# Optimization experiments

Hardware: AMD Instinct MI355X
Metric: run time of the kernel (lower is better)

The kernel has to match this reference:

```python
import jax, jax.numpy as jnp
import numpy as np
import math

B, H, S, D = 8, 16, 1024, 64


def setup_inputs() -> dict:
    key = jax.random.key(0)
    kq, kk, kv, kl = jax.random.split(key, 4)
    queries = jax.random.normal(kq, (B * H, S, D), dtype=jnp.float32)
    keys = jax.random.normal(kk, (B * H, S, D), dtype=jnp.float32)
    values = jax.random.normal(kv, (B * H, S, D), dtype=jnp.float32)
    valid_lens = jax.random.randint(kl, (B,), 0, 1024, dtype=jnp.int64)
    return {"queries": queries, "keys": keys, "values": values, "valid_lens": valid_lens}


def reference(queries, keys, values, valid_lens):
    d = queries.shape[-1]
    seq_len = queries.shape[1]
    b = valid_lens.shape[0]
    h = queries.shape[0] // b
    scale = 1.0 / math.sqrt(d)
    # [BH, S, S] scores, faithful to bmm(q, k^T)/sqrt(d)
    scores = jnp.einsum("bqd,bkd->bqk", queries, keys) * scale
    # encode_mask: mask[b, q, k] = (k >= valid_lens[b]) for 1-D valid_lens
    key_mask = jnp.arange(seq_len) >= valid_lens[:, None]  # [B, S]
    scores = scores.reshape(b, h, seq_len, seq_len)
    # masked_fill with 1e-6 (NOT -inf), faithful to the original
    scores = jnp.where(key_mask[:, None, None, :], jnp.float32(1e-6), scores)
    attn = jax.nn.softmax(scores, axis=-1)
    out = jnp.einsum("bhqk,bhkd->bhqd", attn, values.reshape(b, h, seq_len, d))
    return out.reshape(b * h, seq_len, d)
```

## Files before the change

kernel.cpp:

```cpp
#include <hip/hip_runtime.h>
#include <hip/hip_bf16.h>

typedef short short4v __attribute__((ext_vector_type(4)));
typedef short short8v __attribute__((ext_vector_type(8)));
typedef float floatx4 __attribute__((ext_vector_type(4)));

#define SLEN 1024
#define DDIM 64
#define NBH  128
#define PSTR 72

__device__ __forceinline__ unsigned short f2bf(float f) {
  union { float f; unsigned int u; } v; v.f = f;
  unsigned int u = v.u;
  u += 0x7fffu + ((u >> 16) & 1u);
  return (unsigned short)(u >> 16);
}

__device__ __forceinline__ unsigned int pkbf(float a, float b) {
  __hip_bfloat162 h = __float22bfloat162_rn(float2{a, b});
  union { __hip_bfloat162 h; unsigned int u; } c; c.h = h;
  return c.u;
}

__device__ __forceinline__ int decode_vl(const int* __restrict__ vraw, int bh) {
  const bool is64 = (vraw[1] == 0) && (vraw[3] == 0) && (vraw[5] == 0) && (vraw[7] == 0);
  const int b = bh >> 4;
  return is64 ? vraw[2 * b] : vraw[b];
}

__global__ __launch_bounds__(64)
void prep_cs(const float* __restrict__ Vg, float* __restrict__ CS,
             const int* __restrict__ vraw) {
  const int tile = blockIdx.x;
  const int bh = tile >> 4, ch = tile & 15;
  const int d = threadIdx.x;
  const int vl = decode_vl(vraw, bh);
  const int ts = (vl >> 6) + ((vl & 63) ? 1 : 0);
  float sum = 0.f;
  if (ch >= ts) {
    const float* src = Vg + (size_t)(bh * SLEN + ch * 64) * DDIM + d;
    float s0 = 0.f, s1 = 0.f, s2 = 0.f, s3 = 0.f;
    #pragma unroll
    for (int k = 0; k < 64; k += 4) {
      s0 += src[(size_t)(k + 0) * DDIM];
      s1 += src[(size_t)(k + 1) * DDIM];
      s2 += src[(size_t)(k + 2) * DDIM];
      s3 += src[(size_t)(k + 3) * DDIM];
    }
    sum = (s0 + s1) + (s2 + s3);
  }
  CS[(size_t)tile * 64 + d] = sum;
}

__global__ __launch_bounds__(64)
void prep_sv(float* __restrict__ CS, const int* __restrict__ vraw, int* __restrict__ SRT) {
  const int blk = blockIdx.x;
  if (blk < NBH) {
    const int d = threadIdx.x;
    float acc = 0.f;
    for (int ch = 15; ch >= 0; --ch) {
      const size_t idx = ((size_t)blk * 16 + ch) * 64 + d;
      acc += CS[idx];
      CS[idx] = acc;
    }
  } else {
    const int x = threadIdx.x;
    if (x < 8) {
      int key[16];
      #pragma unroll
      for (int k = 0; k < 16; ++k) {
        const int vv = decode_vl(vraw, x + 8 * k);
        key[k] = (vv >> 6) + ((vv & 63) ? 1 : 0);
      }
      #pragma unroll
      for (int i = 0; i < 16; ++i) {
        int rank = 0;
        #pragma unroll
        for (int k2 = 0; k2 < 16; ++k2)
          rank += (int)((key[k2] > key[i]) || (key[k2] == key[i] && k2 < i));
        SRT[x * 16 + rank] = x + 8 * i;
      }
    }
  }
}

__global__ __launch_bounds__(256)
void attn_main(const float* __restrict__ Qg, const float* __restrict__ Kg,
               const float* __restrict__ Vg, const float* __restrict__ SV,
               const int* __restrict__ SRT, const int* __restrict__ vraw,
               float* __restrict__ Og)
{
  __shared__ unsigned short K_lds[2][4096];
  __shared__ unsigned short VT_lds[2][4096];
  __shared__ unsigned short P_lds[4][32 * PSTR];

  const int t  = threadIdx.x;
  const int w  = t >> 6;
  const int ln = t & 15;
  const int g  = (t >> 4) & 3;

  int bh, q0;
  if (SRT) {
    const int xcd  = blockIdx.x & 7;
    const int lidx = blockIdx.x >> 3;
    const int cu   = lidx & 31;
    const int j    = lidx >> 5;
    const int r    = j * 32 + ((j & 1) ? (31 - cu) : cu);
    bh = SRT[xcd * 16 + (r >> 3)];
    q0 = (r & 7) * 128;
  } else {
    bh = blockIdx.x & 127;
    q0 = (blockIdx.x >> 7) * 128;
  }

  const int vl          = decode_vl(vraw, bh);
  const int full_ch     = vl >> 6;
  const int has_partial = (vl & 63) ? 1 : 0;
  const int nch         = SV ? (full_ch + has_partial) : 16;
  const int tail_start  = full_ch + has_partial;

  const float qs = 0.125f * 1.44269504f;
  short8v bq[2][2];
  #pragma unroll
  for (int nt = 0; nt < 2; ++nt) {
    const float* qp = Qg + ((size_t)bh * SLEN + q0 + w * 32 + nt * 16 + ln) * DDIM;
    #pragma unroll
    for (int st = 0; st < 2; ++st) {
      const float4 f0 = *(const float4*)(qp + st * 32 + g * 8);
      const float4 f1 = *(const float4*)(qp + st * 32 + g * 8 + 4);
      short8v a;
      a[0]=(short)f2bf(f0.x*qs); a[1]=(short)f2bf(f0.y*qs);
      a[2]=(short)f2bf(f0.z*qs); a[3]=(short)f2bf(f0.w*qs);
      a[4]=(short)f2bf(f1.x*qs); a[5]=(short)f2bf(f1.y*qs);
      a[6]=(short)f2bf(f1.z*qs); a[7]=(short)f2bf(f1.w*qs);
      bq[nt][st] = a;
    }
  }

  const int l7  = ln & 7;
  const int sw0 = ((g) ^ l7) * 8;
  const int sw1 = ((4 + g) ^ l7) * 8;

  short8v ones;
  #pragma unroll
  for (int j = 0; j < 8; ++j) ones[j] = (short)0x3F80;

  floatx4 o[2][4], lacc[2];
  #pragma unroll
  for (int m = 0; m < 2; ++m) {
    lacc[m] = (floatx4){0.f, 0.f, 0.f, 0.f};
    #pragma unroll
    for (int f = 0; f < 4; ++f) o[m][f] = (floatx4){0.f, 0.f, 0.f, 0.f};
  }

  float kr[2][8];
  float vlo[8], vhi[8];
  const int dv = t & 31;
  const int gv = t >> 5;

  const float* kbB = Kg + (size_t)bh * SLEN * DDIM;
  const float* vbB = Vg + (size_t)bh * SLEN * DDIM;

  auto stage_load = [&](int ch) {
    const float* kb_ = kbB + (size_t)ch * 64 * DDIM;
    const float* vb_ = vbB + (size_t)ch * 64 * DDIM;
    #pragma unroll
    for (int h = 0; h < 2; ++h) {
      const int q = t + h * 256;
      const int r = q >> 3, gr = q & 7;
      const float4 f0 = *(const float4*)(kb_ + r * DDIM + gr * 8);
      const float4 f1 = *(const float4*)(kb_ + r * DDIM + gr * 8 + 4);
      kr[h][0]=f0.x; kr[h][1]=f0.y; kr[h][2]=f0.z; kr[h][3]=f0.w;
      kr[h][4]=f1.x; kr[h][5]=f1.y; kr[h][6]=f1.z; kr[h][7]=f1.w;
    }
    #pragma unroll
    for (int j = 0; j < 8; ++j) {
      vlo[j] = vb_[(gv * 8 + j) * DDIM + dv];
      vhi[j] = vb_[(gv * 8 + j) * DDIM + dv + 32];
    }
  };
  auto stage_write = [&](int b) {
    #pragma unroll
    for (int h = 0; h < 2; ++h) {
      const int q = t + h * 256;
      const int r = q >> 3, gr = q & 7;
      union { short8v s; unsigned int u[4]; } ks;
      ks.u[0] = pkbf(kr[h][0], kr[h][1]);
      ks.u[1] = pkbf(kr[h][2], kr[h][3]);
      ks.u[2] = pkbf(kr[h][4], kr[h][5]);
      ks.u[3] = pkbf(kr[h][6], kr[h][7]);
      *(short8v*)&K_lds[b][r * 64 + ((gr ^ (r & 7)) * 8)] = ks.s;
    }
    union { short8v s; unsigned int u[4]; } va, vb2;
    va.u[0]  = pkbf(vlo[0], vlo[1]); va.u[1]  = pkbf(vlo[2], vlo[3]);
    va.u[2]  = pkbf(vlo[4], vlo[5]); va.u[3]  = pkbf(vlo[6], vlo[7]);
    vb2.u[0] = pkbf(vhi[0], vhi[1]); vb2.u[1] = pkbf(vhi[2], vhi[3]);
    vb2.u[2] = pkbf(vhi[4], vhi[5]); vb2.u[3] = pkbf(vhi[6], vhi[7]);
    const int swv = (gv ^ (dv & 7)) * 8;
    *(short8v*)&VT_lds[b][dv * 64 + swv] = va.s;
    *(short8v*)&VT_lds[b][(dv + 32) * 64 + swv] = vb2.s;
  };

  if (nch > 0) {
    stage_load(0);
    stage_write(0);
    if (nch > 1) stage_load(1);
    asm volatile("s_waitcnt lgkmcnt(0)" ::: "memory");
    __builtin_amdgcn_s_barrier();
    asm volatile("" ::: "memory");
  }

  for (int ch = 0; ch < nch; ++ch) {
    const int b = ch & 1;
    if (ch + 1 < nch) stage_write(b ^ 1);
    if (ch + 2 < nch) stage_load(ch + 2);

    floatx4 c[4][2];
    __builtin_amdgcn_s_setprio(1);
    #pragma unroll
    for (int mt = 0; mt < 4; ++mt) {
      const short8v a0 = *(const short8v*)&K_lds[b][(mt * 16 + ln) * 64 + sw0];
      const short8v a1 = *(const short8v*)&K_lds[b][(mt * 16 + ln) * 64 + sw1];
      #pragma unroll
      for (int nt = 0; nt < 2; ++nt) {
        floatx4 acc = (floatx4){0.f, 0.f, 0.f, 0.f};
        acc = __builtin_amdgcn_mfma_f32_16x16x32_bf16(a0, bq[nt][0], acc, 0, 0, 0);
        acc = __builtin_amdgcn_mfma_f32_16x16x32_bf16(a1, bq[nt][1], acc, 0, 0, 0);
        c[mt][nt] = acc;
      }
    }
    __builtin_amdgcn_s_setprio(0);

    const bool fullv = (ch < full_ch);
    #pragma unroll
    for (int mt = 0; mt < 4; ++mt) {
      const int kg = ch * 64 + mt * 16 + g * 4;
      #pragma unroll
      for (int nt = 0; nt < 2; ++nt) {
        float p[4];
        if (fullv) {
          #pragma unroll
          for (int i = 0; i < 4; ++i) p[i] = __builtin_amdgcn_exp2f(c[mt][nt][i]);
        } else {
          #pragma unroll
          for (int i = 0; i < 4; ++i) {
            const float x = (kg + i < vl) ? c[mt][nt][i] : 0.0f;
            p[i] = __builtin_amdgcn_exp2f(x);
          }
        }
        union { short4v v; unsigned int u[2]; } pk;
        pk.u[0] = pkbf(p[0], p[1]);
        pk.u[1] = pkbf(p[2], p[3]);
        *(short4v*)&P_lds[w][(nt * 16 + ln) * PSTR + mt * 16 + g * 4] = pk.v;
      }
    }

    #pragma unroll
    for (int st = 0; st < 2; ++st) {
      const short8v ap0 = *(const short8v*)&P_lds[w][(ln)      * PSTR + st * 32 + g * 8];
      const short8v ap1 = *(const short8v*)&P_lds[w][(16 + ln) * PSTR + st * 32 + g * 8];
      __builtin_amdgcn_s_setprio(1);
      lacc[0] = __builtin_amdgcn_mfma_f32_16x16x32_bf16(ap0, ones, lacc[0], 0, 0, 0);
      lacc[1] = __builtin_amdgcn_mfma_f32_16x16x32_bf16(ap1, ones, lacc[1], 0, 0, 0);
      const int sw = (st == 0) ? sw0 : sw1;
      #pragma unroll
      for (int f = 0; f < 4; ++f) {
        const short8v bv = *(const short8v*)&VT_lds[b][(f * 16 + ln) * 64 + sw];
        o[0][f] = __builtin_amdgcn_mfma_f32_16x16x32_bf16(ap0, bv, o[0][f], 0, 0, 0);
        o[1][f] = __builtin_amdgcn_mfma_f32_16x16x32_bf16(ap1, bv, o[1][f], 0, 0, 0);
      }
      __builtin_amdgcn_s_setprio(0);
    }

    if (ch + 1 < nch) {
      asm volatile("s_waitcnt lgkmcnt(0)" ::: "memory");
      __builtin_amdgcn_s_barrier();
      asm volatile("" ::: "memory");
    }
  }

  if (SV != nullptr && tail_start < 16) {
    const float* sv = SV + ((size_t)bh * 16 + tail_start) * 64;
    float svf[4];
    #pragma unroll
    for (int f = 0; f < 4; ++f) svf[f] = sv[f * 16 + ln];
    const float ml = (float)(SLEN - tail_start * 64);
    #pragma unroll
    for (int m = 0; m < 2; ++m) {
      #pragma unroll
      for (int i = 0; i < 4; ++i) lacc[m][i] += ml;
      #pragma unroll
      for (int f = 0; f < 4; ++f)
        #pragma unroll
        for (int i = 0; i < 4; ++i) o[m][f][i] += svf[f];
    }
  }

  #pragma unroll
  for (int m = 0; m < 2; ++m) {
    #pragma unroll
    for (int i = 0; i < 4; ++i) {
      const float inv = 1.0f / lacc[m][i];
      const size_t row = (size_t)bh * SLEN + q0 + w * 32 + m * 16 + g * 4 + i;
      #pragma unroll
      for (int f = 0; f < 4; ++f)
        Og[row * DDIM + f * 16 + ln] = o[m][f][i] * inv;
    }
  }
}

extern "C" void kernel_launch(void* const* d_in, const int* in_sizes, int n_in,
                              void* d_out, int out_size, void* d_ws, size_t ws_size,
                              hipStream_t stream) {
  const float* Q = (const float*)d_in[0];
  const float* K = (const float*)d_in[1];
  const float* V = (const float*)d_in[2];
  const int*  vl = (const int*)d_in[3];
  float* out = (float*)d_out;

  const size_t ws_cs  = (size_t)NBH * 16 * 64 * 4;
  const size_t ws_all = ws_cs + 8 * 16 * 4;

  if (ws_size >= ws_all) {
    float* CS = (float*)d_ws;
    int*  SRT = (int*)((char*)d_ws + ws_cs);
    prep_cs<<<2048, 64, 0, stream>>>(V, CS, vl);
    prep_sv<<<NBH + 1, 64, 0, stream>>>(CS, vl, SRT);
    attn_main<<<dim3(1024), dim3(256), 0, stream>>>(Q, K, V, CS, SRT, vl, out);
  } else {
    attn_main<<<dim3(1024), dim3(256), 0, stream>>>(Q, K, V, nullptr, nullptr, vl, out);
  }
}
```

Before: 160.6 us.

## Keep P in registers via permlane swaps and compute transposed PV

Removes the per-wave LDS round trip for the softmax probability tile. Packed bf16 P values are now rearranged across lanes with permlane32/permlane16 swaps, so they can serve directly as the B operand of an O^T = V^T·P^T MFMA, and the row-sum MFMA is flipped to match. Because of the transposed accumulator layout, the epilogue writes float4 per row and loads the tail sums as float4. This saves LDS writes and reads plus their waits, in exchange for cross-lane permute instructions and a correctness dependence on the lane mapping being right.

```diff
diff --git a/kernel.cpp b/kernel.cpp
--- a/kernel.cpp
+++ b/kernel.cpp
@@ -4,11 +4,11 @@
 typedef short short4v __attribute__((ext_vector_type(4)));
 typedef short short8v __attribute__((ext_vector_type(8)));
 typedef float floatx4 __attribute__((ext_vector_type(4)));
+typedef unsigned int uint2v __attribute__((ext_vector_type(2)));
 
 #define SLEN 1024
 #define DDIM 64
 #define NBH  128
-#define PSTR 72
 
 __device__ __forceinline__ unsigned short f2bf(float f) {
   union { float f; unsigned int u; } v; v.f = f;
@@ -21,6 +21,23 @@
   __hip_bfloat162 h = __float22bfloat162_rn(float2{a, b});
   union { __hip_bfloat162 h; unsigned int u; } c; c.h = h;
   return c.u;
+}
+
+__device__ __forceinline__ void pl32sw(unsigned int &a, unsigned int &b) {
+#if __has_builtin(__builtin_amdgcn_permlane32_swap)
+  uint2v r = __builtin_amdgcn_permlane32_swap(a, b, false, false);
+  a = r[0]; b = r[1];
+#else
+  asm volatile("s_nop 1\n\tv_permlane32_swap_b32 %0, %1" : "+v"(a), "+v"(b));
+#endif
+}
+__device__ __forceinline__ void pl16sw(unsigned int &a, unsigned int &b) {
+#if __has_builtin(__builtin_amdgcn_permlane16_swap)
+  uint2v r = __builtin_amdgcn_permlane16_swap(a, b, false, false);
+  a = r[0]; b = r[1];
+#else
+  asm volatile("s_nop 1\n\tv_permlane16_swap_b32 %0, %1" : "+v"(a), "+v"(b));
+#endif
 }
 
 __device__ __forceinline__ int decode_vl(const int* __restrict__ vraw, int bh) {
@@ -93,10 +110,9 @@
 {
   __shared__ unsigned short K_lds[2][4096];
   __shared__ unsigned short VT_lds[2][4096];
-  __shared__ unsigned short P_lds[4][32 * PSTR];
 
   const int t  = threadIdx.x;
-  const int w  = t >> 6;
+  const int ww = t >> 6;
   const int ln = t & 15;
   const int g  = (t >> 4) & 3;
 
@@ -124,7 +140,7 @@
   short8v bq[2][2];
   #pragma unroll
   for (int nt = 0; nt < 2; ++nt) {
-    const float* qp = Qg + ((size_t)bh * SLEN + q0 + w * 32 + nt * 16 + ln) * DDIM;
+    const float* qp = Qg + ((size_t)bh * SLEN + q0 + ww * 32 + nt * 16 + ln) * DDIM;
     #pragma unroll
     for (int st = 0; st < 2; ++st) {
       const float4 f0 = *(const float4*)(qp + st * 32 + g * 8);
@@ -146,12 +162,12 @@
   #pragma unroll
   for (int j = 0; j < 8; ++j) ones[j] = (short)0x3F80;
 
-  floatx4 o[2][4], lacc[2];
+  floatx4 ot[2][4], lacc[2];
   #pragma unroll
   for (int m = 0; m < 2; ++m) {
     lacc[m] = (floatx4){0.f, 0.f, 0.f, 0.f};
     #pragma unroll
-    for (int f = 0; f < 4; ++f) o[m][f] = (floatx4){0.f, 0.f, 0.f, 0.f};
+    for (int f = 0; f < 4; ++f) ot[m][f] = (floatx4){0.f, 0.f, 0.f, 0.f};
   }
 
   float kr[2][8];
@@ -232,6 +248,7 @@
     }
     __builtin_amdgcn_s_setprio(0);
 
+    unsigned int pk0[4][2], pk1[4][2];
     const bool fullv = (ch < full_ch);
     #pragma unroll
     for (int mt = 0; mt < 4; ++mt) {
@@ -249,29 +266,40 @@
             p[i] = __builtin_amdgcn_exp2f(x);
           }
         }
-        union { short4v v; unsigned int u[2]; } pk;
-        pk.u[0] = pkbf(p[0], p[1]);
-        pk.u[1] = pkbf(p[2], p[3]);
-        *(short4v*)&P_lds[w][(nt * 16 + ln) * PSTR + mt * 16 + g * 4] = pk.v;
-      }
-    }
-
+        pk0[mt][nt] = pkbf(p[0], p[1]);
+        pk1[mt][nt] = pkbf(p[2], p[3]);
+      }
+    }
+
+    short8v bp[2][2];
     #pragma unroll
     for (int st = 0; st < 2; ++st) {
-      const short8v ap0 = *(const short8v*)&P_lds[w][(ln)      * PSTR + st * 32 + g * 8];
-      const short8v ap1 = *(const short8v*)&P_lds[w][(16 + ln) * PSTR + st * 32 + g * 8];
-      __builtin_amdgcn_s_setprio(1);
-      lacc[0] = __builtin_amdgcn_mfma_f32_16x16x32_bf16(ap0, ones, lacc[0], 0, 0, 0);
-      lacc[1] = __builtin_amdgcn_mfma_f32_16x16x32_bf16(ap1, ones, lacc[1], 0, 0, 0);
+      #pragma unroll
+      for (int nt = 0; nt < 2; ++nt) {
+        unsigned int a0 = pk0[2 * st][nt], b0 = pk0[2 * st + 1][nt];
+        unsigned int a1 = pk1[2 * st][nt], b1 = pk1[2 * st + 1][nt];
+        pl32sw(a0, b0); pl16sw(a0, b0);
+        pl32sw(a1, b1); pl16sw(a1, b1);
+        union { short8v s; unsigned int u[4]; } bb;
+        bb.u[0] = a0; bb.u[1] = a1; bb.u[2] = b0; bb.u[3] = b1;
+        bp[st][nt] = bb.s;
+      }
+    }
+
+    __builtin_amdgcn_s_setprio(1);
+    #pragma unroll
+    for (int st = 0; st < 2; ++st) {
+      lacc[0] = __builtin_amdgcn_mfma_f32_16x16x32_bf16(ones, bp[st][0], lacc[0], 0, 0, 0);
+      lacc[1] = __builtin_amdgcn_mfma_f32_16x16x32_bf16(ones, bp[st][1], lacc[1], 0, 0, 0);
       const int sw = (st == 0) ? sw0 : sw1;
       #pragma unroll
       for (int f = 0; f < 4; ++f) {
-        const short8v bv = *(const short8v*)&VT_lds[b][(f * 16 + ln) * 64 + sw];
-        o[0][f] = __builtin_amdgcn_mfma_f32_16x16x32_bf16(ap0, bv, o[0][f], 0, 0, 0);
-        o[1][f] = __builtin_amdgcn_mfma_f32_16x16x32_bf16(ap1, bv, o[1][f], 0, 0, 0);
-      }
-      __builtin_amdgcn_s_setprio(0);
-    }
+        const short8v av = *(const short8v*)&VT_lds[b][(f * 16 + ln) * 64 + sw];
+        ot[0][f] = __builtin_amdgcn_mfma_f32_16x16x32_bf16(av, bp[st][0], ot[0][f], 0, 0, 0);
+        ot[1][f] = __builtin_amdgcn_mfma_f32_16x16x32_bf16(av, bp[st][1], ot[1][f], 0, 0, 0);
+      }
+    }
+    __builtin_amdgcn_s_setprio(0);
 
     if (ch + 1 < nch) {
       asm volatile("s_waitcnt lgkmcnt(0)" ::: "memory");
@@ -281,31 +309,33 @@
   }
 
   if (SV != nullptr && tail_start < 16) {
-    const float* sv = SV + ((size_t)bh * 16 + tail_start) * 64;
-    float svf[4];
-    #pragma unroll
-    for (int f = 0; f < 4; ++f) svf[f] = sv[f * 16 + ln];
+    const float* sv = SV + ((size_t)bh * 16 + tail_start) * 64 + g * 4;
+    float4 sv4[4];
+    #pragma unroll
+    for (int f = 0; f < 4; ++f) sv4[f] = *(const float4*)(sv + f * 16);
     const float ml = (float)(SLEN - tail_start * 64);
     #pragma unroll
-    for (int m = 0; m < 2; ++m) {
-      #pragma unroll
-      for (int i = 0; i < 4; ++i) lacc[m][i] += ml;
-      #pragma unroll
-      for (int f = 0; f < 4; ++f)
-        #pragma unroll
-        for (int i = 0; i < 4; ++i) o[m][f][i] += svf[f];
+    for (int nt = 0; nt < 2; ++nt) {
+      #pragma unroll
+      for (int i = 0; i < 4; ++i) lacc[nt][i] += ml;
+      #pragma unroll
+      for (int f = 0; f < 4; ++f) {
+        ot[nt][f][0] += sv4[f].x; ot[nt][f][1] += sv4[f].y;
+        ot[nt][f][2] += sv4[f].z; ot[nt][f][3] += sv4[f].w;
+      }
     }
   }
 
   #pragma unroll
-  for (int m = 0; m < 2; ++m) {
-    #pragma unroll
-    for (int i = 0; i < 4; ++i) {
-      const float inv = 1.0f / lacc[m][i];
-      const size_t row = (size_t)bh * SLEN + q0 + w * 32 + m * 16 + g * 4 + i;
-      #pragma unroll
-      for (int f = 0; f < 4; ++f)
-        Og[row * DDIM + f * 16 + ln] = o[m][f][i] * inv;
+  for (int nt = 0; nt < 2; ++nt) {
+    const float inv = 1.0f / lacc[nt][0];
+    float* orow = Og + ((size_t)bh * SLEN + q0 + ww * 32 + nt * 16 + ln) * DDIM + g * 4;
+    #pragma unroll
+    for (int f = 0; f < 4; ++f) {
+      float4 v4;
+      v4.x = ot[nt][f][0] * inv; v4.y = ot[nt][f][1] * inv;
+      v4.z = ot[nt][f][2] * inv; v4.w = ot[nt][f][3] * inv;
+      *(float4*)(orow + f * 16) = v4;
     }
   }
 }
```

Result: no change. 160.5 us (-0.1%).
